# Optimization experiments

Measured on AMD Instinct MI355X. Metric: run time of the kernel, lower is better.

## Reference

```python
import jax, jax.numpy as jnp
import numpy as np

N_TX, N_ADDR = 100000, 150000
E = 1500000
F_TX, F_ADDR = 165, 64
HID, H, EMB = 32, 2, 64
HO = HID * H  # 64, concat-heads output dim
NEG_SLOPE = 0.2


def _edge_softmax(logits, dst, num_dst):
    # logits: [E, H]; softmax over edges sharing the same destination node
    m = jax.ops.segment_max(logits, dst, num_segments=num_dst)
    e = jnp.exp(logits - m[dst])
    s = jax.ops.segment_sum(e, dst, num_segments=num_dst)
    return e / (s[dst] + 1e-16)


def _gat(x_src, x_dst, src, dst, W, a_s, a_d, b, num_dst):
    # PyG GATConv (add_self_loops=False, concat=True): shared lin for src/dst
    hs = (x_src @ W).reshape(-1, H, HID)  # [Ns, H, C]
    hd = (x_dst @ W).reshape(-1, H, HID)  # [Nd, H, C]
    al_s = (hs * a_s).sum(-1)             # [Ns, H]
    al_d = (hd * a_d).sum(-1)             # [Nd, H]
    logit = jax.nn.leaky_relu(al_s[src] + al_d[dst], NEG_SLOPE)  # [E, H]
    alpha = _edge_softmax(logit, dst, num_dst)                    # [E, H]
    msg = hs[src] * alpha[:, :, None]                             # [E, H, C]
    out = jax.ops.segment_sum(msg, dst, num_segments=num_dst)    # [Nd, H, C]
    return out.reshape(num_dst, HO) + b


def _ln(x, g, b):
    mu = jnp.mean(x, -1, keepdims=True)
    v = jnp.var(x, -1, keepdims=True)
    return (x - mu) * jax.lax.rsqrt(v + 1e-5) * g + b


def _forward(floats, ints):
    (x_tx, x_addr, Wp_tx, bp_tx, Wp_addr, bp_addr,
     W_ta0, as_ta0, ad_ta0, b_ta0, W_at0, as_at0, ad_at0, b_at0,
     W_ta1, as_ta1, ad_ta1, b_ta1, W_at1, as_at1, ad_at1, b_at1,
     g_tx, be_tx, g_addr, be_addr, Wo, bo) = floats
    e_src_ta, e_dst_ta, e_src_at, e_dst_at = ints

    tx = x_tx @ Wp_tx + bp_tx        # [N_TX, HID]
    ad = x_addr @ Wp_addr + bp_addr  # [N_ADDR, HID]

    layer_params = [
        (W_ta0, as_ta0, ad_ta0, b_ta0, W_at0, as_at0, ad_at0, b_at0),
        (W_ta1, as_ta1, ad_ta1, b_ta1, W_at1, as_at1, ad_at1, b_at1),
    ]
    for (Wta, asta, adta, bta, Wat, asat, adat, bat) in layer_params:
        # HeteroConv with aggr='sum': each ntype receives from exactly one relation
        new_ad = _gat(tx, ad, e_src_ta, e_dst_ta, Wta, asta, adta, bta, N_ADDR)
        new_tx = _gat(ad, tx, e_src_at, e_dst_at, Wat, asat, adat, bat, N_TX)
        ntx = _ln(new_tx, g_tx, be_tx)
        if tx.shape == ntx.shape:  # residual only when shapes match (layer >= 1)
            ntx = ntx + tx
        nad = _ln(new_ad, g_addr, be_addr)
        if ad.shape == nad.shape:
            nad = nad + ad
        tx = jax.nn.elu(ntx)  # dropout is identity in eval mode
        ad = jax.nn.elu(nad)

    return tx @ Wo + bo  # [N_TX, EMB]


def setup_inputs() -> dict:
    key = jax.random.key(0)
    ks = iter(jax.random.split(key, 40))
    rn = lambda shape, s=0.1: jax.random.normal(next(ks), shape, dtype=jnp.float32) * s
    ri = lambda shape, hi: jax.random.randint(next(ks), shape, 0, hi, dtype=jnp.int32)
    d = {}
    d['x_tx'] = rn((N_TX, F_TX), 1.0)
    d['x_addr'] = rn((N_ADDR, F_ADDR), 1.0)
    d['Wp_tx'] = rn((F_TX, HID)); d['bp_tx'] = jnp.zeros((HID,), jnp.float32)
    d['Wp_addr'] = rn((F_ADDR, HID)); d['bp_addr'] = jnp.zeros((HID,), jnp.float32)
    for li, ind in ((0, HID), (1, HO)):
        for rel in ('ta', 'at'):
            d['W_%s%d' % (rel, li)] = rn((ind, HO))
            d['as_%s%d' % (rel, li)] = rn((H, HID))
            d['ad_%s%d' % (rel, li)] = rn((H, HID))
            d['b_%s%d' % (rel, li)] = jnp.zeros((HO,), jnp.float32)
    d['g_tx'] = jnp.ones((HO,), jnp.float32); d['be_tx'] = jnp.zeros((HO,), jnp.float32)
    d['g_addr'] = jnp.ones((HO,), jnp.float32); d['be_addr'] = jnp.zeros((HO,), jnp.float32)
    d['Wo'] = rn((HO, EMB)); d['bo'] = jnp.zeros((EMB,), jnp.float32)
    d['e_src_ta'] = ri((E,), N_TX); d['e_dst_ta'] = ri((E,), N_ADDR)
    d['e_src_at'] = ri((E,), N_ADDR); d['e_dst_at'] = ri((E,), N_TX)
    return d


def reference(x_tx, x_addr, Wp_tx, bp_tx, Wp_addr, bp_addr,
              W_ta0, as_ta0, ad_ta0, b_ta0, W_at0, as_at0, ad_at0, b_at0,
              W_ta1, as_ta1, ad_ta1, b_ta1, W_at1, as_at1, ad_at1, b_at1,
              g_tx, be_tx, g_addr, be_addr, Wo, bo,
              e_src_ta, e_dst_ta, e_src_at, e_dst_at):
    floats = (x_tx, x_addr, Wp_tx, bp_tx, Wp_addr, bp_addr,
              W_ta0, as_ta0, ad_ta0, b_ta0, W_at0, as_at0, ad_at0, b_at0,
              W_ta1, as_ta1, ad_ta1, b_ta1, W_at1, as_at1, ad_at1, b_at1,
              g_tx, be_tx, g_addr, be_addr, Wo, bo)
    ints = (e_src_ta, e_dst_ta, e_src_at, e_dst_at)
    return _forward(floats, ints)
```

## Files before the change

kernel.cpp:

```cpp
#include <hip/hip_runtime.h>
#include <hip/hip_bf16.h>
#include <math.h>

static constexpr int kNTx   = 100000;
static constexpr int kNAddr = 150000;
static constexpr int kE     = 1500000;
static constexpr int kFTx   = 165;
static constexpr int kFAddr = 64;
static constexpr int kHid   = 32;
static constexpr int kHO    = 64;

template<int K>
__global__ void proj_kernel(const float* __restrict__ X, const float* __restrict__ W,
                            const float* __restrict__ bias, float* __restrict__ out, int N) {
  __shared__ float Wl[K * kHid];
  for (int i = threadIdx.x; i < K * kHid; i += blockDim.x) Wl[i] = W[i];
  __syncthreads();
  int row = blockIdx.x * (blockDim.x / kHid) + threadIdx.x / kHid;
  int col = threadIdx.x % kHid;
  if (row >= N) return;
  const float* xr = X + (size_t)row * K;
  float acc = 0.f;
  #pragma unroll 5
  for (int k = 0; k < K; ++k) acc = fmaf(xr[k], Wl[k * kHid + col], acc);
  out[(size_t)row * kHid + col] = acc + bias[col];
}

template<int K>
__global__ void hs_als_kernel(const float* __restrict__ X, const float* __restrict__ W,
                              const float* __restrict__ a_s,
                              float* __restrict__ HS, float* __restrict__ ALS, int N) {
  __shared__ float Wl[K * kHO];
  __shared__ float asl[kHO];
  for (int i = threadIdx.x; i < K * kHO; i += blockDim.x) Wl[i] = W[i];
  if (threadIdx.x < kHO) asl[threadIdx.x] = a_s[threadIdx.x];
  __syncthreads();
  int row = blockIdx.x * (blockDim.x >> 6) + (threadIdx.x >> 6);
  int col = threadIdx.x & 63;
  if (row >= N) return;
  const float* xr = X + (size_t)row * K;
  float acc = 0.f;
  #pragma unroll 8
  for (int k = 0; k < K; ++k) acc = fmaf(xr[k], Wl[k * kHO + col], acc);
  HS[(size_t)row * kHO + col] = acc;
  float p = acc * asl[col];
  for (int off = 16; off >= 1; off >>= 1) p += __shfl_xor(p, off);
  if ((col & 31) == 0) ALS[(size_t)row * 2 + (col >> 5)] = p;
}

template<int K>
__global__ void ald_kernel(const float* __restrict__ X, const float* __restrict__ W,
                           const float* __restrict__ a_d, float* __restrict__ ALD, int N) {
  __shared__ float Vd[K * 2];
  __shared__ float adl[kHO];
  if (threadIdx.x < kHO) adl[threadIdx.x] = a_d[threadIdx.x];
  __syncthreads();
  for (int i = threadIdx.x; i < K * 2; i += blockDim.x) {
    int k = i >> 1, h = i & 1;
    float s = 0.f;
    #pragma unroll
    for (int c = 0; c < kHid; ++c) s = fmaf(W[k * kHO + h * kHid + c], adl[h * kHid + c], s);
    Vd[i] = s;
  }
  __syncthreads();
  int row = blockIdx.x * (blockDim.x >> 1) + (threadIdx.x >> 1);
  int h = threadIdx.x & 1;
  if (row >= N) return;
  const float* xr = X + (size_t)row * K;
  float acc = 0.f;
  #pragma unroll 8
  for (int k = 0; k < K; ++k) acc = fmaf(xr[k], Vd[k * 2 + h], acc);
  ALD[(size_t)row * 2 + h] = acc;
}

__global__ void count_kernel(const int* __restrict__ dst, int* __restrict__ cnt, int E) {
  int i = blockIdx.x * blockDim.x + threadIdx.x;
  if (i < E) atomicAdd(&cnt[dst[i]], 1);
}

static constexpr int kScanChunk = 2048;

__global__ void scan1_kernel(const int* __restrict__ in, int* __restrict__ out,
                             int* __restrict__ bsums, int N) {
  __shared__ int sm[256];
  int base = blockIdx.x * kScanChunk + threadIdx.x * 8;
  int v[8];
  int ls = 0;
  #pragma unroll
  for (int j = 0; j < 8; ++j) {
    int idx = base + j;
    int x = (idx < N) ? in[idx] : 0;
    v[j] = x; ls += x;
  }
  sm[threadIdx.x] = ls;
  __syncthreads();
  for (int off = 1; off < 256; off <<= 1) {
    int t = (threadIdx.x >= off) ? sm[threadIdx.x - off] : 0;
    __syncthreads();
    sm[threadIdx.x] += t;
    __syncthreads();
  }
  int excl = sm[threadIdx.x] - ls;
  if (threadIdx.x == 255) bsums[blockIdx.x] = sm[255];
  int run = excl;
  #pragma unroll
  for (int j = 0; j < 8; ++j) {
    int idx = base + j;
    if (idx < N) out[idx] = run;
    run += v[j];
  }
}

__global__ void scan2_kernel(int* __restrict__ bsums, int nb) {
  if (blockIdx.x == 0 && threadIdx.x == 0) {
    int run = 0;
    for (int i = 0; i < nb; ++i) { int t = bsums[i]; bsums[i] = run; run += t; }
  }
}

__global__ void scan3_kernel(int* __restrict__ out, const int* __restrict__ bsums,
                             int N, int total) {
  int add = bsums[blockIdx.x];
  int base = blockIdx.x * kScanChunk + threadIdx.x * 8;
  #pragma unroll
  for (int j = 0; j < 8; ++j) {
    int idx = base + j;
    if (idx < N) out[idx] += add;
  }
  if (blockIdx.x == 0 && threadIdx.x == 0) out[N] = total;
}

__global__ void scatter_kernel(const int* __restrict__ src, const int* __restrict__ dst,
                               const int* __restrict__ offs, int* __restrict__ cur,
                               int* __restrict__ csrc, int E) {
  int i = blockIdx.x * blockDim.x + threadIdx.x;
  if (i < E) {
    int d = dst[i];
    int pos = atomicAdd(&cur[d], 1);
    csrc[offs[d] + pos] = src[i];
  }
}

__global__ void gat_agg_kernel(const int* __restrict__ offs, const int* __restrict__ csrc,
                               const float* __restrict__ HS, const float* __restrict__ ALS,
                               const float* __restrict__ ALD, const float* __restrict__ bias,
                               float* __restrict__ out, int Nd) {
  int wave = threadIdx.x >> 6;
  int lane = threadIdx.x & 63;
  int dst = blockIdx.x * (blockDim.x >> 6) + wave;
  if (dst >= Nd) return;
  int h = lane >> 5, c = lane & 31;
  int beg = offs[dst], end = offs[dst + 1];
  float bval = bias[lane];
  if (beg == end) {
    out[(size_t)dst * kHO + lane] = bval;
    return;
  }
  float aldh = ALD[(size_t)dst * 2 + h];
  float m = -INFINITY, s = 0.f;
  for (int i = beg + c; i < end; i += 32) {
    int sv = csrc[i];
    float logit = ALS[(size_t)sv * 2 + h] + aldh;
    logit = logit > 0.f ? logit : 0.2f * logit;
    if (logit > m) { s = s * __expf(m - logit) + 1.f; m = logit; }
    else            s += __expf(logit - m);
  }
  for (int off = 16; off >= 1; off >>= 1) {
    float mo = __shfl_xor(m, off);
    float so = __shfl_xor(s, off);
    float mn = fmaxf(m, mo);
    float sa = (m  == -INFINITY) ? 0.f : s  * __expf(m  - mn);
    float sb = (mo == -INFINITY) ? 0.f : so * __expf(mo - mn);
    m = mn; s = sa + sb;
  }
  float inv_denom = 1.f / (s + 1e-16f);
  float acc = 0.f;
  for (int i = beg; i < end; ++i) {
    int sv = csrc[i];
    float logit = ALS[(size_t)sv * 2 + h] + aldh;
    logit = logit > 0.f ? logit : 0.2f * logit;
    float alpha = __expf(logit - m) * inv_denom;
    acc = fmaf(alpha, HS[(size_t)sv * kHO + lane], acc);
  }
  out[(size_t)dst * kHO + lane] = acc + bval;
}

__global__ void ln_kernel(const float* __restrict__ X, const float* __restrict__ g,
                          const float* __restrict__ be, const float* __restrict__ res,
                          float* __restrict__ out, int N, int use_res) {
  int row = blockIdx.x * (blockDim.x >> 6) + (threadIdx.x >> 6);
  int lane = threadIdx.x & 63;
  if (row >= N) return;
  float x = X[(size_t)row * kHO + lane];
  float sum = x, sq = x * x;
  for (int off = 32; off >= 1; off >>= 1) {
    sum += __shfl_xor(sum, off);
    sq  += __shfl_xor(sq, off);
  }
  float mu = sum * (1.f / kHO);
  float var = sq * (1.f / kHO) - mu * mu;
  float y = (x - mu) * rsqrtf(var + 1e-5f) * g[lane] + be[lane];
  if (use_res) y += res[(size_t)row * kHO + lane];
  out[(size_t)row * kHO + lane] = y > 0.f ? y : expm1f(y);
}

__global__ void outproj_kernel(const float* __restrict__ X, const float* __restrict__ W,
                               const float* __restrict__ bias, float* __restrict__ out, int N) {
  __shared__ float Wl[kHO * kHO];
  for (int i = threadIdx.x; i < kHO * kHO; i += blockDim.x) Wl[i] = W[i];
  __syncthreads();
  int row = blockIdx.x * (blockDim.x >> 6) + (threadIdx.x >> 6);
  int col = threadIdx.x & 63;
  if (row >= N) return;
  const float* xr = X + (size_t)row * kHO;
  float acc = 0.f;
  #pragma unroll
  for (int k = 0; k < kHO; ++k) acc = fmaf(xr[k], Wl[k * kHO + col], acc);
  out[(size_t)row * kHO + col] = acc + bias[col];
}

extern "C" void kernel_launch(void* const* d_in, const int* in_sizes, int n_in,
                              void* d_out, int out_size, void* d_ws, size_t ws_size,
                              hipStream_t stream) {
  const float* x_tx    = (const float*)d_in[0];
  const float* x_addr  = (const float*)d_in[1];
  const float* Wp_tx   = (const float*)d_in[2];
  const float* bp_tx   = (const float*)d_in[3];
  const float* Wp_addr = (const float*)d_in[4];
  const float* bp_addr = (const float*)d_in[5];
  const float* W_ta0   = (const float*)d_in[6];
  const float* as_ta0  = (const float*)d_in[7];
  const float* ad_ta0  = (const float*)d_in[8];
  const float* b_ta0   = (const float*)d_in[9];
  const float* W_at0   = (const float*)d_in[10];
  const float* as_at0  = (const float*)d_in[11];
  const float* ad_at0  = (const float*)d_in[12];
  const float* b_at0   = (const float*)d_in[13];
  const float* W_ta1   = (const float*)d_in[14];
  const float* as_ta1  = (const float*)d_in[15];
  const float* ad_ta1  = (const float*)d_in[16];
  const float* b_ta1   = (const float*)d_in[17];
  const float* W_at1   = (const float*)d_in[18];
  const float* as_at1  = (const float*)d_in[19];
  const float* ad_at1  = (const float*)d_in[20];
  const float* b_at1   = (const float*)d_in[21];
  const float* g_tx    = (const float*)d_in[22];
  const float* be_tx   = (const float*)d_in[23];
  const float* g_addr  = (const float*)d_in[24];
  const float* be_addr = (const float*)d_in[25];
  const float* Wo      = (const float*)d_in[26];
  const float* bo      = (const float*)d_in[27];
  const int* e_src_ta  = (const int*)d_in[28];
  const int* e_dst_ta  = (const int*)d_in[29];
  const int* e_src_at  = (const int*)d_in[30];
  const int* e_dst_at  = (const int*)d_in[31];
  (void)in_sizes; (void)n_in; (void)out_size; (void)ws_size;

  char* p = (char*)d_ws;
  auto alloc = [&](size_t bytes) { char* r = p; p += (bytes + 255) & ~(size_t)255; return r; };
  float* txp  = (float*)alloc((size_t)kNTx   * kHid * 4);
  float* adp  = (float*)alloc((size_t)kNAddr * kHid * 4);
  float* txf  = (float*)alloc((size_t)kNTx   * kHO * 4);
  float* adf  = (float*)alloc((size_t)kNAddr * kHO * 4);
  float* hs   = (float*)alloc((size_t)kNAddr * kHO * 4);
  float* aggA = (float*)alloc((size_t)kNAddr * kHO * 4);
  float* aggT = (float*)alloc((size_t)kNTx   * kHO * 4);
  float* als  = (float*)alloc((size_t)kNAddr * 2 * 4);
  float* ald  = (float*)alloc((size_t)kNAddr * 2 * 4);
  int* offs_ta = (int*)alloc((size_t)(kNAddr + 1) * 4);
  int* cur_ta  = (int*)alloc((size_t)kNAddr * 4);
  int* srcs_ta = (int*)alloc((size_t)kE * 4);
  int* offs_at = (int*)alloc((size_t)(kNTx + 1) * 4);
  int* cur_at  = (int*)alloc((size_t)kNTx * 4);
  int* srcs_at = (int*)alloc((size_t)kE * 4);
  int* bsums   = (int*)alloc(1024 * 4);

  const int EB = (kE + 255) / 256;

  auto build_csr = [&](const int* esrc, const int* edst, int Nd,
                       int* offs, int* cur, int* csrc) {
    hipMemsetAsync(cur, 0, (size_t)Nd * 4, stream);
    count_kernel<<<EB, 256, 0, stream>>>(edst, cur, kE);
    int nb = (Nd + kScanChunk - 1) / kScanChunk;
    scan1_kernel<<<nb, 256, 0, stream>>>(cur, offs, bsums, Nd);
    scan2_kernel<<<1, 64, 0, stream>>>(bsums, nb);
    scan3_kernel<<<nb, 256, 0, stream>>>(offs, bsums, Nd, kE);
    hipMemsetAsync(cur, 0, (size_t)Nd * 4, stream);
    scatter_kernel<<<EB, 256, 0, stream>>>(esrc, edst, offs, cur, csrc, kE);
  };
  build_csr(e_src_ta, e_dst_ta, kNAddr, offs_ta, cur_ta, srcs_ta);
  build_csr(e_src_at, e_dst_at, kNTx,   offs_at, cur_at, srcs_at);

  proj_kernel<kFTx><<<(kNTx + 7) / 8, 256, 0, stream>>>(x_tx, Wp_tx, bp_tx, txp, kNTx);
  proj_kernel<kFAddr><<<(kNAddr + 7) / 8, 256, 0, stream>>>(x_addr, Wp_addr, bp_addr, adp, kNAddr);

  hs_als_kernel<kHid><<<(kNTx + 3) / 4, 256, 0, stream>>>(txp, W_ta0, as_ta0, hs, als, kNTx);
  ald_kernel<kHid><<<(kNAddr + 127) / 128, 256, 0, stream>>>(adp, W_ta0, ad_ta0, ald, kNAddr);
  gat_agg_kernel<<<(kNAddr + 3) / 4, 256, 0, stream>>>(offs_ta, srcs_ta, hs, als, ald, b_ta0, aggA, kNAddr);
  hs_als_kernel<kHid><<<(kNAddr + 3) / 4, 256, 0, stream>>>(adp, W_at0, as_at0, hs, als, kNAddr);
  ald_kernel<kHid><<<(kNTx + 127) / 128, 256, 0, stream>>>(txp, W_at0, ad_at0, ald, kNTx);
  gat_agg_kernel<<<(kNTx + 3) / 4, 256, 0, stream>>>(offs_at, srcs_at, hs, als, ald, b_at0, aggT, kNTx);
  ln_kernel<<<(kNTx + 3) / 4, 256, 0, stream>>>(aggT, g_tx, be_tx, txf, txf, kNTx, 0);
  ln_kernel<<<(kNAddr + 3) / 4, 256, 0, stream>>>(aggA, g_addr, be_addr, adf, adf, kNAddr, 0);

  hs_als_kernel<kHO><<<(kNTx + 3) / 4, 256, 0, stream>>>(txf, W_ta1, as_ta1, hs, als, kNTx);
  ald_kernel<kHO><<<(kNAddr + 127) / 128, 256, 0, stream>>>(adf, W_ta1, ad_ta1, ald, kNAddr);
  gat_agg_kernel<<<(kNAddr + 3) / 4, 256, 0, stream>>>(offs_ta, srcs_ta, hs, als, ald, b_ta1, aggA, kNAddr);
  hs_als_kernel<kHO><<<(kNAddr + 3) / 4, 256, 0, stream>>>(adf, W_at1, as_at1, hs, als, kNAddr);
  ald_kernel<kHO><<<(kNTx + 127) / 128, 256, 0, stream>>>(txf, W_at1, ad_at1, ald, kNTx);
  gat_agg_kernel<<<(kNTx + 3) / 4, 256, 0, stream>>>(offs_at, srcs_at, hs, als, ald, b_at1, aggT, kNTx);
  ln_kernel<<<(kNTx + 3) / 4, 256, 0, stream>>>(aggT, g_tx, be_tx, txf, txf, kNTx, 1);
  ln_kernel<<<(kNAddr + 3) / 4, 256, 0, stream>>>(aggA, g_addr, be_addr, adf, adf, kNAddr, 1);

  outproj_kernel<<<(kNTx + 3) / 4, 256, 0, stream>>>(txf, Wo, bo, (float*)d_out, kNTx);
}
```

Before: 1.893 ms.

## Fuse source and destination attention projections per node type and unroll aggregation gathers

After: 1.923 ms. No clear change (+1.6%).

```diff
diff --git a/kernel.cpp b/kernel.cpp
--- a/kernel.cpp
+++ b/kernel.cpp
@@ -27,50 +27,47 @@
 }
 
 template<int K>
-__global__ void hs_als_kernel(const float* __restrict__ X, const float* __restrict__ W,
-                              const float* __restrict__ a_s,
-                              float* __restrict__ HS, float* __restrict__ ALS, int N) {
+__global__ void node_feats_kernel(const float* __restrict__ X,
+                                  const float* __restrict__ W, const float* __restrict__ a_s,
+                                  const float* __restrict__ Wother, const float* __restrict__ a_d,
+                                  float* __restrict__ HS, float* __restrict__ ALS,
+                                  float* __restrict__ ALD, int N) {
   __shared__ float Wl[K * kHO];
+  __shared__ float vd[K * 2];
   __shared__ float asl[kHO];
   for (int i = threadIdx.x; i < K * kHO; i += blockDim.x) Wl[i] = W[i];
   if (threadIdx.x < kHO) asl[threadIdx.x] = a_s[threadIdx.x];
+  for (int i = threadIdx.x; i < K * 2; i += blockDim.x) {
+    int k = i >> 1, hh = i & 1;
+    float s = 0.f;
+    #pragma unroll
+    for (int c = 0; c < kHid; ++c)
+      s = fmaf(Wother[k * kHO + hh * kHid + c], a_d[hh * kHid + c], s);
+    vd[i] = s;
+  }
   __syncthreads();
   int row = blockIdx.x * (blockDim.x >> 6) + (threadIdx.x >> 6);
-  int col = threadIdx.x & 63;
+  int lane = threadIdx.x & 63;
   if (row >= N) return;
   const float* xr = X + (size_t)row * K;
+  float xv = (lane < K) ? xr[lane] : 0.f;
+  float p0 = (lane < K) ? xv * vd[lane * 2 + 0] : 0.f;
+  float p1 = (lane < K) ? xv * vd[lane * 2 + 1] : 0.f;
+  for (int off = 32; off >= 1; off >>= 1) {
+    p0 += __shfl_xor(p0, off);
+    p1 += __shfl_xor(p1, off);
+  }
+  if (lane == 0) {
+    ALD[(size_t)row * 2 + 0] = p0;
+    ALD[(size_t)row * 2 + 1] = p1;
+  }
   float acc = 0.f;
   #pragma unroll 8
-  for (int k = 0; k < K; ++k) acc = fmaf(xr[k], Wl[k * kHO + col], acc);
-  HS[(size_t)row * kHO + col] = acc;
-  float p = acc * asl[col];
+  for (int k = 0; k < K; ++k) acc = fmaf(xr[k], Wl[k * kHO + lane], acc);
+  HS[(size_t)row * kHO + lane] = acc;
+  float p = acc * asl[lane];
   for (int off = 16; off >= 1; off >>= 1) p += __shfl_xor(p, off);
-  if ((col & 31) == 0) ALS[(size_t)row * 2 + (col >> 5)] = p;
-}
-
-template<int K>
-__global__ void ald_kernel(const float* __restrict__ X, const float* __restrict__ W,
-                           const float* __restrict__ a_d, float* __restrict__ ALD, int N) {
-  __shared__ float Vd[K * 2];
-  __shared__ float adl[kHO];
-  if (threadIdx.x < kHO) adl[threadIdx.x] = a_d[threadIdx.x];
-  __syncthreads();
-  for (int i = threadIdx.x; i < K * 2; i += blockDim.x) {
-    int k = i >> 1, h = i & 1;
-    float s = 0.f;
-    #pragma unroll
-    for (int c = 0; c < kHid; ++c) s = fmaf(W[k * kHO + h * kHid + c], adl[h * kHid + c], s);
-    Vd[i] = s;
-  }
-  __syncthreads();
-  int row = blockIdx.x * (blockDim.x >> 1) + (threadIdx.x >> 1);
-  int h = threadIdx.x & 1;
-  if (row >= N) return;
-  const float* xr = X + (size_t)row * K;
-  float acc = 0.f;
-  #pragma unroll 8
-  for (int k = 0; k < K; ++k) acc = fmaf(xr[k], Vd[k * 2 + h], acc);
-  ALD[(size_t)row * 2 + h] = acc;
+  if ((lane & 31) == 0) ALS[(size_t)row * 2 + (lane >> 5)] = p;
 }
 
 __global__ void count_kernel(const int* __restrict__ dst, int* __restrict__ cnt, int E) {
@@ -174,13 +171,25 @@
     m = mn; s = sa + sb;
   }
   float inv_denom = 1.f / (s + 1e-16f);
+  constexpr int U = 8;
   float acc = 0.f;
-  for (int i = beg; i < end; ++i) {
-    int sv = csrc[i];
-    float logit = ALS[(size_t)sv * 2 + h] + aldh;
-    logit = logit > 0.f ? logit : 0.2f * logit;
-    float alpha = __expf(logit - m) * inv_denom;
-    acc = fmaf(alpha, HS[(size_t)sv * kHO + lane], acc);
+  for (int base = beg; base < end; base += U) {
+    int sv[U];
+    float al[U];
+    #pragma unroll
+    for (int j = 0; j < U; ++j) {
+      int idx = base + j;
+      sv[j] = csrc[idx < end ? idx : end - 1];
+    }
+    #pragma unroll
+    for (int j = 0; j < U; ++j) {
+      float logit = ALS[(size_t)sv[j] * 2 + h] + aldh;
+      logit = logit > 0.f ? logit : 0.2f * logit;
+      al[j] = (base + j) < end ? __expf(logit - m) * inv_denom : 0.f;
+    }
+    #pragma unroll
+    for (int j = 0; j < U; ++j)
+      acc = fmaf(al[j], HS[(size_t)sv[j] * kHO + lane], acc);
   }
   out[(size_t)dst * kHO + lane] = acc + bval;
 }
@@ -258,15 +267,18 @@
 
   char* p = (char*)d_ws;
   auto alloc = [&](size_t bytes) { char* r = p; p += (bytes + 255) & ~(size_t)255; return r; };
-  float* txp  = (float*)alloc((size_t)kNTx   * kHid * 4);
-  float* adp  = (float*)alloc((size_t)kNAddr * kHid * 4);
-  float* txf  = (float*)alloc((size_t)kNTx   * kHO * 4);
-  float* adf  = (float*)alloc((size_t)kNAddr * kHO * 4);
-  float* hs   = (float*)alloc((size_t)kNAddr * kHO * 4);
-  float* aggA = (float*)alloc((size_t)kNAddr * kHO * 4);
-  float* aggT = (float*)alloc((size_t)kNTx   * kHO * 4);
-  float* als  = (float*)alloc((size_t)kNAddr * 2 * 4);
-  float* ald  = (float*)alloc((size_t)kNAddr * 2 * 4);
+  float* txp   = (float*)alloc((size_t)kNTx   * kHid * 4);
+  float* adp   = (float*)alloc((size_t)kNAddr * kHid * 4);
+  float* txf   = (float*)alloc((size_t)kNTx   * kHO * 4);
+  float* adf   = (float*)alloc((size_t)kNAddr * kHO * 4);
+  float* hsTA  = (float*)alloc((size_t)kNTx   * kHO * 4);
+  float* hsAT  = (float*)alloc((size_t)kNAddr * kHO * 4);
+  float* aggA  = (float*)alloc((size_t)kNAddr * kHO * 4);
+  float* aggT  = (float*)alloc((size_t)kNTx   * kHO * 4);
+  float* alsTA = (float*)alloc((size_t)kNTx   * 2 * 4);
+  float* aldAT = (float*)alloc((size_t)kNTx   * 2 * 4);
+  float* alsAT = (float*)alloc((size_t)kNAddr * 2 * 4);
+  float* aldTA = (float*)alloc((size_t)kNAddr * 2 * 4);
   int* offs_ta = (int*)alloc((size_t)(kNAddr + 1) * 4);
   int* cur_ta  = (int*)alloc((size_t)kNAddr * 4);
   int* srcs_ta = (int*)alloc((size_t)kE * 4);
@@ -294,21 +306,25 @@
   proj_kernel<kFTx><<<(kNTx + 7) / 8, 256, 0, stream>>>(x_tx, Wp_tx, bp_tx, txp, kNTx);
   proj_kernel<kFAddr><<<(kNAddr + 7) / 8, 256, 0, stream>>>(x_addr, Wp_addr, bp_addr, adp, kNAddr);
 
-  hs_als_kernel<kHid><<<(kNTx + 3) / 4, 256, 0, stream>>>(txp, W_ta0, as_ta0, hs, als, kNTx);
-  ald_kernel<kHid><<<(kNAddr + 127) / 128, 256, 0, stream>>>(adp, W_ta0, ad_ta0, ald, kNAddr);
-  gat_agg_kernel<<<(kNAddr + 3) / 4, 256, 0, stream>>>(offs_ta, srcs_ta, hs, als, ald, b_ta0, aggA, kNAddr);
-  hs_als_kernel<kHid><<<(kNAddr + 3) / 4, 256, 0, stream>>>(adp, W_at0, as_at0, hs, als, kNAddr);
-  ald_kernel<kHid><<<(kNTx + 127) / 128, 256, 0, stream>>>(txp, W_at0, ad_at0, ald, kNTx);
-  gat_agg_kernel<<<(kNTx + 3) / 4, 256, 0, stream>>>(offs_at, srcs_at, hs, als, ald, b_at0, aggT, kNTx);
+  node_feats_kernel<kHid><<<(kNTx + 3) / 4, 256, 0, stream>>>(
+      txp, W_ta0, as_ta0, W_at0, ad_at0, hsTA, alsTA, aldAT, kNTx);
+  node_feats_kernel<kHid><<<(kNAddr + 3) / 4, 256, 0, stream>>>(
+      adp, W_at0, as_at0, W_ta0, ad_ta0, hsAT, alsAT, aldTA, kNAddr);
+  gat_agg_kernel<<<(kNAddr + 3) / 4, 256, 0, stream>>>(
+      offs_ta, srcs_ta, hsTA, alsTA, aldTA, b_ta0, aggA, kNAddr);
+  gat_agg_kernel<<<(kNTx + 3) / 4, 256, 0, stream>>>(
+      offs_at, srcs_at, hsAT, alsAT, aldAT, b_at0, aggT, kNTx);
   ln_kernel<<<(kNTx + 3) / 4, 256, 0, stream>>>(aggT, g_tx, be_tx, txf, txf, kNTx, 0);
   ln_kernel<<<(kNAddr + 3) / 4, 256, 0, stream>>>(aggA, g_addr, be_addr, adf, adf, kNAddr, 0);
 
-  hs_als_kernel<kHO><<<(kNTx + 3) / 4, 256, 0, stream>>>(txf, W_ta1, as_ta1, hs, als, kNTx);
-  ald_kernel<kHO><<<(kNAddr + 127) / 128, 256, 0, stream>>>(adf, W_ta1, ad_ta1, ald, kNAddr);
-  gat_agg_kernel<<<(kNAddr + 3) / 4, 256, 0, stream>>>(offs_ta, srcs_ta, hs, als, ald, b_ta1, aggA, kNAddr);
-  hs_als_kernel<kHO><<<(kNAddr + 3) / 4, 256, 0, stream>>>(adf, W_at1, as_at1, hs, als, kNAddr);
-  ald_kernel<kHO><<<(kNTx + 127) / 128, 256, 0, stream>>>(txf, W_at1, ad_at1, ald, kNTx);
-  gat_agg_kernel<<<(kNTx + 3) / 4, 256, 0, stream>>>(offs_at, srcs_at, hs, als, ald, b_at1, aggT, kNTx);
+  node_feats_kernel<kHO><<<(kNTx + 3) / 4, 256, 0, stream>>>(
+      txf, W_ta1, as_ta1, W_at1, ad_at1, hsTA, alsTA, aldAT, kNTx);
+  node_feats_kernel<kHO><<<(kNAddr + 3) / 4, 256, 0, stream>>>(
+      adf, W_at1, as_at1, W_ta1, ad_ta1, hsAT, alsAT, aldTA, kNAddr);
+  gat_agg_kernel<<<(kNAddr + 3) / 4, 256, 0, stream>>>(
+      offs_ta, srcs_ta, hsTA, alsTA, aldTA, b_ta1, aggA, kNAddr);
+  gat_agg_kernel<<<(kNTx + 3) / 4, 256, 0, stream>>>(
+      offs_at, srcs_at, hsAT, alsAT, aldAT, b_at1, aggT, kNTx);
   ln_kernel<<<(kNTx + 3) / 4, 256, 0, stream>>>(aggT, g_tx, be_tx, txf, txf, kNTx, 1);
   ln_kernel<<<(kNAddr + 3) / 4, 256, 0, stream>>>(aggA, g_addr, be_addr, adf, adf, kNAddr, 1);
 
```
